# Kernel tuning notes

Measured on AMD Instinct MI355X. Metric: run time of the kernel, lower is better.

Reference implementation:

```python
import jax, jax.numpy as jnp
import numpy as np

N = 100000       # total_nodes
E = 400000       # total_events (event == E, all events used)
EMBED = 128
HIDDEN = 128
CLASSES = 10
Q = 4096         # query pairs for link prediction
BN_EPS = 1e-5


def _bn(x):
    # BatchNorm1d(affine=False), training mode: biased variance over batch dim
    m = jnp.mean(x, axis=0)
    var = jnp.var(x, axis=0)
    return (x - m) * jax.lax.rsqrt(var + BN_EPS)


def _t2_layer(h, u, v, g, w1, w2):
    # per-edge source features: [h[dst-side], g]  -> scatter_add into (N, F)
    src_u = jnp.concatenate([h[u], g], axis=1)   # (E, F)
    src_v = jnp.concatenate([h[v], g], axis=1)   # (E, F)
    F = src_u.shape[1]
    agg = (jnp.zeros((N, F), h.dtype)
           .at[v].add(src_u)
           .at[u].add(src_v))                    # agg_u + agg_v fused
    z = jax.nn.relu(_bn(agg) @ w1.T)             # (N, F)
    return jnp.concatenate([h, z], axis=1) @ w2.T  # (N, F + prev_embed)


def setup_inputs() -> dict:
    key = jax.random.key(0)
    ks = jax.random.split(key, 14)
    s = 0.05
    return {
        "u": jax.random.randint(ks[0], (E,), 0, N, dtype=jnp.int32),
        "v": jax.random.randint(ks[1], (E,), 0, N, dtype=jnp.int32),
        "t": jnp.sort(jax.random.uniform(ks[2], (E,), dtype=jnp.float32)),
        "qu": jax.random.randint(ks[3], (Q,), 0, N, dtype=jnp.int32),
        "qv": jax.random.randint(ks[4], (Q,), 0, N, dtype=jnp.int32),
        "h0": jax.random.uniform(ks[5], (N, EMBED), dtype=jnp.float32),
        "w1_0": jax.random.normal(ks[6], (129, 129), jnp.float32) * s,
        "w2_0": jax.random.normal(ks[7], (257, 257), jnp.float32) * s,
        "w1_1": jax.random.normal(ks[8], (258, 258), jnp.float32) * s,
        "w2_1": jax.random.normal(ks[9], (515, 515), jnp.float32) * s,
        "link_h": jax.random.normal(ks[10], (HIDDEN, 2 * 515), jnp.float32) * s,
        "link_o": jax.random.normal(ks[11], (1, HIDDEN), jnp.float32) * s,
        "node_h": jax.random.normal(ks[12], (HIDDEN, 515), jnp.float32) * s,
        "node_o": jax.random.normal(ks[13], (CLASSES, HIDDEN), jnp.float32) * s,
    }


def reference(u, v, t, qu, qv, h0, w1_0, w2_0, w1_1, w2_1,
              link_h, link_o, node_h, node_o):
    # g = (tlast - t) / (1 + tlast - tfirst), shape (E, 1)
    g = ((t[-1] - t) / (1.0 + t[-1] - t[0]))[:, None]
    h = _t2_layer(h0, u, v, g, w1_0, w2_0)   # (N, 257)
    h = _t2_layer(h, u, v, g, w1_1, w2_1)    # (N, 515)
    # link prediction head on query pairs
    hq = jnp.concatenate([h[qu], h[qv]], axis=1)            # (Q, 1030)
    link = (jax.nn.relu(hq @ link_h.T) @ link_o.T)[:, 0]    # (Q,)
    # node prediction head
    node = jax.nn.relu(h @ node_h.T) @ node_o.T             # (N, CLASSES)
    return link, node
```

## Files before the change

kernel.cpp:

```cpp
#include <hip/hip_runtime.h>
#include <hip/hip_bf16.h>

#define NN      100000
#define EE      400000
#define QQ      4096
#define CLASSES 10
#define BN_EPS  1e-5f
#define NCHUNK  256

typedef __hip_bfloat16 bf16;
typedef __attribute__((ext_vector_type(8))) short short8v;
typedef __attribute__((ext_vector_type(4))) float float4v;

__device__ inline float ldv(const float* p, long i) { return p[i]; }
__device__ inline float ldv(const bf16*  p, long i) { return __bfloat162float(p[i]); }
__device__ inline void  stv(float* p, long i, float v) { p[i] = v; }
__device__ inline void  stv(bf16*  p, long i, float v) { p[i] = __float2bfloat16(v); }

__device__ inline unsigned short f2b(float f) { bf16 b = __float2bfloat16(f); unsigned short s; __builtin_memcpy(&s, &b, 2); return s; }
__device__ inline float b2f(unsigned short s) { bf16 b; __builtin_memcpy(&b, &s, 2); return __bfloat162float(b); }

__device__ __forceinline__ void gload_lds16(const void* g, void* l) {
    __builtin_amdgcn_global_load_lds(
        (const __attribute__((address_space(1))) void*)g,
        (__attribute__((address_space(3))) void*)l,
        16, 0, 0);
}

__global__ void zero_kernel(float* __restrict__ p, size_t n) {
    size_t i  = (size_t)blockIdx.x * blockDim.x + threadIdx.x;
    size_t st = (size_t)gridDim.x * blockDim.x;
    for (; i < n; i += st) p[i] = 0.f;
}

__global__ void csr_count_kernel(const int* __restrict__ u, const int* __restrict__ v, int E, int* __restrict__ deg) {
    int e = blockIdx.x * 256 + threadIdx.x;
    if (e < E) { atomicAdd(&deg[u[e]], 1); atomicAdd(&deg[v[e]], 1); }
}

__global__ __launch_bounds__(256) void csr_chunksum_kernel(const int* __restrict__ deg, int N, int chunk, int* __restrict__ bsum) {
    __shared__ int sh[256];
    int b = blockIdx.x, tid = threadIdx.x;
    int i0 = b * chunk, i1 = min(N, i0 + chunk);
    int s = 0;
    for (int i = i0 + tid; i < i1; i += 256) s += deg[i];
    sh[tid] = s; __syncthreads();
    for (int st = 128; st > 0; st >>= 1) { if (tid < st) sh[tid] += sh[tid + st]; __syncthreads(); }
    if (tid == 0) bsum[b] = sh[0];
}

__global__ void csr_scanb_kernel(const int* __restrict__ bsum, int* __restrict__ boff) {
    if (threadIdx.x == 0 && blockIdx.x == 0) {
        int r = 0;
        for (int i = 0; i < NCHUNK; ++i) { boff[i] = r; r += bsum[i]; }
    }
}

__global__ void csr_rowp_kernel(const int* __restrict__ deg, const int* __restrict__ boff,
                                int N, int chunk, int* __restrict__ rowp, int* __restrict__ cur) {
    int b = blockIdx.x;
    if (threadIdx.x != 0) return;
    int i0 = b * chunk, i1 = min(N, i0 + chunk);
    int r = boff[b];
    for (int i = i0; i < i1; ++i) { rowp[i] = r; cur[i] = r; r += deg[i]; }
    if (b == NCHUNK - 1) rowp[N] = r;
}

__global__ void csr_fill_kernel(const int* __restrict__ u, const int* __restrict__ v,
                                const float* __restrict__ t, int E,
                                int* __restrict__ cur, int* __restrict__ adj, float* __restrict__ gsum) {
    int e = blockIdx.x * 256 + threadIdx.x;
    if (e >= E) return;
    int a = u[e], b = v[e];
    float tlast = t[E - 1], tfirst = t[0];
    float ge = (tlast - t[e]) / (1.0f + tlast - tfirst);
    int p = atomicAdd(&cur[a], 1); adj[p] = b;
    int q = atomicAdd(&cur[b], 1); adj[q] = a;
    atomicAdd(&gsum[a], ge); atomicAdd(&gsum[b], ge);
}

__global__ __launch_bounds__(256) void gather_l1_kernel(
    const float* __restrict__ h0, const int* __restrict__ rowp, const int* __restrict__ adj,
    const float* __restrict__ gsum, bf16* __restrict__ out, int N)
{
    int n = blockIdx.x * 4 + (threadIdx.x >> 6);
    if (n >= N) return;
    int lane = threadIdx.x & 63;
    float a0 = 0.f, a1 = 0.f;
    int j0 = rowp[n], j1 = rowp[n + 1];
    for (int j = j0; j < j1; ++j) {
        int o = adj[j];
        const float2 x = *(const float2*)(h0 + (long)o * 128 + 2 * lane);
        a0 += x.x; a1 += x.y;
    }
    bf16* orow = out + (long)n * 136;
    ushort2 pv; pv.x = f2b(a0); pv.y = f2b(a1);
    ((ushort2*)orow)[lane] = pv;
    if (lane == 0) {
        orow[128] = __float2bfloat16(gsum[n]);
        orow[129] = __float2bfloat16(0.f);
    } else if (lane < 4) {
        ushort2 z; z.x = 0; z.y = 0;
        ((ushort2*)(orow + 130))[lane - 1] = z;
    }
}

__global__ __launch_bounds__(256) void gather_l2_kernel(
    const bf16* __restrict__ h1, const int* __restrict__ rowp, const int* __restrict__ adj,
    const float* __restrict__ gsum, bf16* __restrict__ out, int N)
{
    int n = blockIdx.x * 4 + (threadIdx.x >> 6);
    if (n >= N) return;
    int lane = threadIdx.x & 63;
    float a0 = 0.f, a1 = 0.f, b0 = 0.f, b1 = 0.f, cS = 0.f;
    int j0 = rowp[n], j1 = rowp[n + 1];
    for (int j = j0; j < j1; ++j) {
        int o = adj[j];
        const ushort2* hr = (const ushort2*)(h1 + (long)o * 264);
        ushort2 x = hr[lane];
        ushort2 y = hr[64 + lane];
        a0 += b2f(x.x); a1 += b2f(x.y);
        b0 += b2f(y.x); b1 += b2f(y.y);
        if (lane == 0) cS += __bfloat162float(h1[(long)o * 264 + 256]);
    }
    bf16* orow = out + (long)n * 264;
    ushort2 p0; p0.x = f2b(a0); p0.y = f2b(a1);
    ushort2 p1; p1.x = f2b(b0); p1.y = f2b(b1);
    ((ushort2*)orow)[lane] = p0;
    ((ushort2*)orow)[64 + lane] = p1;
    if (lane == 0) {
        orow[256] = __float2bfloat16(cS);
        orow[257] = __float2bfloat16(gsum[n]);
    } else if (lane < 4) {
        ushort2 z; z.x = 0; z.y = 0;
        ((ushort2*)orow)[128 + lane] = z;
    }
}

__global__ __launch_bounds__(256) void col_stats_b_kernel(
    const bf16* __restrict__ X, int ld, int Nrows, int F,
    float* __restrict__ sum, float* __restrict__ sumsq)
{
    int tid = threadIdx.x;
    int rpb = (Nrows + gridDim.x - 1) / gridDim.x;
    int r0 = blockIdx.x * rpb, r1 = min(Nrows, r0 + rpb);
    int c0 = tid, c1 = tid + 256;
    float s0 = 0.f, q0 = 0.f, s1 = 0.f, q1 = 0.f;
    for (int r = r0; r < r1; ++r) {
        const bf16* row = X + (long)r * ld;
        if (c0 < F) { float x = __bfloat162float(row[c0]); s0 += x; q0 += x * x; }
        if (c1 < F) { float x = __bfloat162float(row[c1]); s1 += x; q1 += x * x; }
    }
    if (c0 < F) { atomicAdd(&sum[c0], s0); atomicAdd(&sumsq[c0], q0); }
    if (c1 < F) { atomicAdd(&sum[c1], s1); atomicAdd(&sumsq[c1], q1); }
}

__global__ void bn_finalize_kernel(const float* __restrict__ sum, const float* __restrict__ sumsq,
                                   int F, float Nf, float* __restrict__ mean, float* __restrict__ scale)
{
    int c = blockIdx.x * blockDim.x + threadIdx.x;
    if (c < F) {
        float m = sum[c] / Nf;
        float var = sumsq[c] / Nf - m * m;
        mean[c] = m;
        scale[c] = 1.0f / sqrtf(var + BN_EPS);
    }
}

__global__ __launch_bounds__(256) void wfold_kernel(
    const float* __restrict__ w, int Ktot, int M,
    const float* __restrict__ mean, const float* __restrict__ scale,
    int Kpad, int Mpad, bf16* __restrict__ wout, float* __restrict__ bias)
{
    __shared__ float sh[256];
    int m = blockIdx.x;
    int tid = threadIdx.x;
    float bs = 0.f;
    bf16* orow = wout + (long)m * Kpad;
    for (int k = tid; k < Kpad; k += 256) {
        float val = 0.f;
        if (m < M && k < Ktot) {
            float wv = w[(long)m * Ktot + k];
            val = wv * scale[k];
            bs -= mean[k] * scale[k] * wv;
        }
        orow[k] = __float2bfloat16(val);
    }
    sh[tid] = bs; __syncthreads();
    for (int st = 128; st > 0; st >>= 1) { if (tid < st) sh[tid] += sh[tid + st]; __syncthreads(); }
    if (tid == 0 && m < M) bias[m] = sh[0];
}

__global__ void wprep_kernel(const float* __restrict__ w, int Ktot, int M,
                             int K1, int W1, int K2, int Kpad, int Mpad,
                             bf16* __restrict__ out)
{
    int idx = blockIdx.x * 256 + threadIdx.x;
    if (idx >= Mpad * Kpad) return;
    int m = idx / Kpad, k = idx - m * Kpad;
    float val = 0.f;
    if (m < M) {
        if (k < W1) { if (k < K1) val = w[(long)m * Ktot + k]; }
        else { int j = k - W1; if (j < K2) val = w[(long)m * Ktot + K1 + j]; }
    }
    out[idx] = __float2bfloat16(val);
}

template<typename CT>
__global__ __launch_bounds__(256) void mfma_gemm_kernel(
    const bf16* __restrict__ A0, int lda0, int W1,
    const bf16* __restrict__ A1, int lda1,
    const bf16* __restrict__ Wb, int Kpad,
    const float* __restrict__ bias,
    CT* __restrict__ C, long ldc, int Nrows, int M, int padlim, int relu)
{
    __shared__ bf16 sA[128 * 32];
    __shared__ bf16 sB[128 * 32];

    int tid  = threadIdx.x;
    int row0 = blockIdx.x * 128;
    int col0 = blockIdx.y * 128;
    int wave = tid >> 6, lane = tid & 63;
    int wr = (wave >> 1) * 64, wc = (wave & 1) * 64;
    int la = lane & 15, hk = lane >> 4;

    float4v acc[4][4];
    #pragma unroll
    for (int i = 0; i < 4; ++i)
        #pragma unroll
        for (int j = 0; j < 4; ++j)
            acc[i][j] = (float4v){0.f, 0.f, 0.f, 0.f};

    const short8v* sA8 = (const short8v*)sA;
    const short8v* sB8 = (const short8v*)sB;

    for (int k0 = 0; k0 < Kpad; k0 += 32) {
        #pragma unroll
        for (int h = 0; h < 2; ++h) {
            int c = tid + h * 256;
            int r = c >> 2, kq = c & 3;
            int ka = k0 + kq * 8;
            int ga_row = row0 + r; if (ga_row >= Nrows) ga_row = Nrows - 1;
            const bf16* gp = (ka < W1) ? (A0 + (long)ga_row * lda0 + ka)
                                       : (A1 + (long)ga_row * lda1 + (ka - W1));
            gload_lds16(gp, (char*)sA + (size_t)c * 16);
            const bf16* gq = Wb + (long)(col0 + r) * Kpad + ka;
            gload_lds16(gq, (char*)sB + (size_t)c * 16);
        }
        __syncthreads();

        short8v afr[4], bfr[4];
        #pragma unroll
        for (int mf = 0; mf < 4; ++mf)
            afr[mf] = sA8[(size_t)(wr + mf * 16 + la) * 4 + hk];
        #pragma unroll
        for (int nf = 0; nf < 4; ++nf)
            bfr[nf] = sB8[(size_t)(wc + nf * 16 + la) * 4 + hk];
        #pragma unroll
        for (int mf = 0; mf < 4; ++mf)
            #pragma unroll
            for (int nf = 0; nf < 4; ++nf)
                acc[mf][nf] = __builtin_amdgcn_mfma_f32_16x16x32_bf16(
                    afr[mf], bfr[nf], acc[mf][nf], 0, 0, 0);
        __syncthreads();
    }

    #pragma unroll
    for (int mf = 0; mf < 4; ++mf) {
        #pragma unroll
        for (int r = 0; r < 4; ++r) {
            long grow = row0 + wr + mf * 16 + hk * 4 + r;
            if (grow >= Nrows) continue;
            #pragma unroll
            for (int nf = 0; nf < 4; ++nf) {
                int gcol = col0 + wc + nf * 16 + la;
                if (gcol >= padlim) continue;
                float vv = 0.f;
                if (gcol < M) {
                    vv = acc[mf][nf][r];
                    if (bias) vv += bias[gcol];
                    if (relu) vv = fmaxf(vv, 0.f);
                }
                stv(C, grow * ldc + gcol, vv);
            }
        }
    }
}

__global__ __launch_bounds__(256) void link_gather_kernel(
    const bf16* __restrict__ h2, const int* __restrict__ qu, const int* __restrict__ qv,
    bf16* __restrict__ hq)
{
    int q = blockIdx.x * 4 + (threadIdx.x >> 6);
    if (q >= QQ) return;
    int lane = threadIdx.x & 63;
    const ushort4* ra4 = (const ushort4*)(h2 + (long)qu[q] * 520);
    const ushort4* rb4 = (const ushort4*)(h2 + (long)qv[q] * 520);
    ushort4* o4 = (ushort4*)(hq + (long)q * 1056);
    #pragma unroll 3
    for (int k = lane; k < 130; k += 64) o4[k] = ra4[k];
    #pragma unroll 3
    for (int k = lane; k < 130; k += 64) o4[130 + k] = rb4[k];
    if (lane < 4) { ushort4 z; z.x = z.y = z.z = z.w = 0; o4[260 + lane] = z; }
}

__global__ __launch_bounds__(256) void link_dot_kernel(
    const float* __restrict__ tmpl, const float* __restrict__ link_o, float* __restrict__ out)
{
    int q = blockIdx.x * 4 + (threadIdx.x >> 6);
    if (q >= QQ) return;
    int lane = threadIdx.x & 63;
    const float* r = tmpl + (long)q * 128;
    float s = r[lane] * link_o[lane] + r[lane + 64] * link_o[lane + 64];
    #pragma unroll
    for (int off = 32; off > 0; off >>= 1) s += __shfl_xor(s, off, 64);
    if (lane == 0) out[q] = s;
}

template<typename HT>
__global__ __launch_bounds__(256) void scatter_edges_kernel(
    const HT* __restrict__ h, int ldh, int P,
    const int* __restrict__ u, const int* __restrict__ v,
    const float* __restrict__ t, int E,
    float* __restrict__ agg, int lda)
{
    long gid = (long)blockIdx.x * blockDim.x + threadIdx.x;
    int e = (int)(gid >> 6);
    int lane = (int)(gid & 63);
    if (e >= E) return;
    int uu = u[e], vv = v[e];
    float tlast = t[E - 1], tfirst = t[0];
    float ge = (tlast - t[e]) / (1.0f + tlast - tfirst);
    const HT* hu = h + (long)uu * ldh;
    const HT* hv = h + (long)vv * ldh;
    float* au = agg + (long)uu * lda;
    float* av = agg + (long)vv * lda;
    for (int f = lane; f < P; f += 64) {
        atomicAdd(&av[f], ldv(hu, f));
        atomicAdd(&au[f], ldv(hv, f));
    }
    if (lane == 0) {
        atomicAdd(&av[P], ge);
        atomicAdd(&au[P], ge);
    }
}

__global__ __launch_bounds__(256) void col_stats_kernel(
    const float* __restrict__ X, int Nrows, int F,
    float* __restrict__ sum, float* __restrict__ sumsq)
{
    int tid = threadIdx.x;
    int rowsPerBlock = (Nrows + gridDim.x - 1) / gridDim.x;
    int r0 = blockIdx.x * rowsPerBlock;
    int r1 = min(Nrows, r0 + rowsPerBlock);
    int c0 = tid, c1 = tid + 256;
    float s0 = 0.f, q0 = 0.f, s1 = 0.f, q1 = 0.f;
    for (int r = r0; r < r1; ++r) {
        const float* row = X + (long)r * F;
        if (c0 < F) { float x = row[c0]; s0 += x; q0 += x * x; }
        if (c1 < F) { float x = row[c1]; s1 += x; q1 += x * x; }
    }
    if (c0 < F) { atomicAdd(&sum[c0], s0); atomicAdd(&sumsq[c0], q0); }
    if (c1 < F) { atomicAdd(&sum[c1], s1); atomicAdd(&sumsq[c1], q1); }
}

#define BM 64
#define BNT 64
#define BK 32
template<typename AT0, typename AT1, typename CT>
__global__ __launch_bounds__(256) void gemm_kernel(
    const AT0* __restrict__ A0, int lda0, int cols0,
    const AT1* __restrict__ A1, int lda1,
    const float* __restrict__ Bw,
    CT* __restrict__ C, int ldc,
    int Nrows, int K, int M,
    const float* __restrict__ bn_mean, const float* __restrict__ bn_scale,
    int relu)
{
    __shared__ float sA[BM][BK + 1];
    __shared__ float sB[BNT][BK + 1];
    int row0 = blockIdx.x * BM;
    int col0 = blockIdx.y * BNT;
    int tid = threadIdx.x;
    int tx = tid & 15, ty = tid >> 4;
    float acc[4][4] = {{0.f}};
    for (int k0 = 0; k0 < K; k0 += BK) {
        int i = tid >> 2;
        int j = (tid & 3) * 8;
        int gr = row0 + i;
        int gm = col0 + i;
        #pragma unroll
        for (int s = 0; s < 8; ++s) {
            int gk = k0 + j + s;
            float val = 0.f;
            if (gr < Nrows && gk < K) {
                if (gk < cols0) val = ldv(A0, (long)gr * lda0 + gk);
                else            val = ldv(A1, (long)gr * lda1 + (gk - cols0));
                if (bn_mean) val = (val - bn_mean[gk]) * bn_scale[gk];
            }
            sA[i][j + s] = val;
            float bv = 0.f;
            if (gm < M && gk < K) bv = Bw[(long)gm * K + gk];
            sB[i][j + s] = bv;
        }
        __syncthreads();
        #pragma unroll
        for (int kk = 0; kk < BK; ++kk) {
            float a[4], b[4];
            #pragma unroll
            for (int r = 0; r < 4; ++r) a[r] = sA[ty * 4 + r][kk];
            #pragma unroll
            for (int c = 0; c < 4; ++c) b[c] = sB[tx * 4 + c][kk];
            #pragma unroll
            for (int r = 0; r < 4; ++r)
                #pragma unroll
                for (int c = 0; c < 4; ++c)
                    acc[r][c] += a[r] * b[c];
        }
        __syncthreads();
    }
    #pragma unroll
    for (int r = 0; r < 4; ++r) {
        int gr = row0 + ty * 4 + r;
        if (gr >= Nrows) continue;
        #pragma unroll
        for (int c = 0; c < 4; ++c) {
            int gm = col0 + tx * 4 + c;
            if (gm >= M) continue;
            float vv = acc[r][c];
            if (relu) vv = fmaxf(vv, 0.f);
            stv(C, (long)gr * ldc + gm, vv);
        }
    }
}

template<typename HT>
__global__ __launch_bounds__(128) void link_kernel(
    const HT* __restrict__ h2, int ldh,
    const int* __restrict__ qu, const int* __restrict__ qv,
    const float* __restrict__ link_h,
    const float* __restrict__ link_o,
    float* __restrict__ out)
{
    __shared__ float sh[1030];
    __shared__ float red[128];
    int q = blockIdx.x;
    int tid = threadIdx.x;
    int a = qu[q], b = qv[q];
    for (int k = tid; k < 515; k += 128) sh[k] = ldv(h2, (long)a * ldh + k);
    for (int k = tid; k < 515; k += 128) sh[515 + k] = ldv(h2, (long)b * ldh + k);
    __syncthreads();
    const float* wrow = link_h + (long)tid * 1030;
    float y = 0.f;
    for (int k = 0; k < 1030; ++k) y += sh[k] * wrow[k];
    y = fmaxf(y, 0.f) * link_o[tid];
    red[tid] = y;
    __syncthreads();
    for (int s = 64; s > 0; s >>= 1) {
        if (tid < s) red[tid] += red[tid + s];
        __syncthreads();
    }
    if (tid == 0) out[q] = red[0];
}

extern "C" void kernel_launch(void* const* d_in, const int* in_sizes, int n_in,
                              void* d_out, int out_size, void* d_ws, size_t ws_size,
                              hipStream_t stream)
{
    const int*   u      = (const int*)d_in[0];
    const int*   v      = (const int*)d_in[1];
    const float* t      = (const float*)d_in[2];
    const int*   qu     = (const int*)d_in[3];
    const int*   qv     = (const int*)d_in[4];
    const float* h0     = (const float*)d_in[5];
    const float* w1_0   = (const float*)d_in[6];
    const float* w2_0   = (const float*)d_in[7];
    const float* w1_1   = (const float*)d_in[8];
    const float* w2_1   = (const float*)d_in[9];
    const float* link_h = (const float*)d_in[10];
    const float* link_o = (const float*)d_in[11];
    const float* node_h = (const float*)d_in[12];
    const float* node_o = (const float*)d_in[13];

    float* out_link = (float*)d_out;
    float* out_node = (float*)d_out + QQ;

    char* wsb = (char*)d_ws;

    float* stats = (float*)wsb;
    float* sum1 = stats,         * sumsq1 = stats + 512;
    float* mean1 = stats + 1024, * scale1 = stats + 1536;
    float* sum2 = stats + 2048,  * sumsq2 = stats + 2560;
    float* mean2 = stats + 3072, * scale2 = stats + 3584;

    if (ws_size >= 217000000ull) {
        bf16* wf1_0 = (bf16*)(wsb + 16384);
        bf16* wb2_0 = (bf16*)(wsb + 98304);
        bf16* wf1_1 = (bf16*)(wsb + 319488);
        bf16* wb2_1 = (bf16*)(wsb + 540672);
        bf16* wbnh  = (bf16*)(wsb + 1236992);
        bf16* wbno  = (bf16*)(wsb + 1376256);
        float* bias1 = (float*)(wsb + 1409024);
        float* bias2 = (float*)(wsb + 1410048);
        float* gsum = (float*)(wsb + 1412096);
        int*   deg  = (int*)  (wsb + 1812096);
        int*   rowp = (int*)  (wsb + 2212096);
        int*   cur  = (int*)  (wsb + 2612104);
        int*   bsum = (int*)  (wsb + 3012104);
        int*   boff = (int*)  (wsb + 3013128);
        int*   adj  = (int*)  (wsb + 3016200);
        bf16*  wlk  = (bf16*) (wsb + 6220000);
        bf16* h1   = (bf16*)(wsb + 6500000ull);
        bf16* tmpb = (bf16*)(wsb + 6500000ull);
        bf16* z0   = (bf16*)(wsb + 59300000ull);
        bf16* h0b  = (bf16*)(wsb + 86500000ull);
        bf16* z1   = (bf16*)(wsb + 59300000ull);
        bf16* hq   = (bf16*)(wsb + 59300000ull);
        float* tmpl = (float*)(wsb + 70000000ull);
        bf16* aggb = (bf16*)(wsb + 112100000ull);
        bf16* h2   = (bf16*)(wsb + 112100000ull);

        const int gx = (NN + 127) / 128;
        const int chunk = (NN + NCHUNK - 1) / NCHUNK;

        zero_kernel<<<16, 256, 0, stream>>>(stats, 4096);
        zero_kernel<<<64, 256, 0, stream>>>(gsum, 200000);

        wprep_kernel<<<432, 256, 0, stream>>>(w2_0, 257, 257, 128, 128, 129, 288, 384, wb2_0);
        wprep_kernel<<<1360, 256, 0, stream>>>(w2_1, 515, 515, 257, 272, 258, 544, 640, wb2_1);
        wprep_kernel<<<272, 256, 0, stream>>>(node_h, 515, 128, 515, 544, 0, 544, 128, wbnh);
        wprep_kernel<<<64, 256, 0, stream>>>(node_o, 128, 10, 128, 128, 0, 128, 128, wbno);
        wprep_kernel<<<528, 256, 0, stream>>>(link_h, 1030, 128, 515, 520, 515, 1056, 128, wlk);

        csr_count_kernel<<<(EE + 255) / 256, 256, 0, stream>>>(u, v, EE, deg);
        csr_chunksum_kernel<<<NCHUNK, 256, 0, stream>>>(deg, NN, chunk, bsum);
        csr_scanb_kernel<<<1, 64, 0, stream>>>(bsum, boff);
        csr_rowp_kernel<<<NCHUNK, 64, 0, stream>>>(deg, boff, NN, chunk, rowp, cur);
        csr_fill_kernel<<<(EE + 255) / 256, 256, 0, stream>>>(u, v, t, EE, cur, adj, gsum);

        gather_l1_kernel<<<NN / 4, 256, 0, stream>>>(h0, rowp, adj, gsum, aggb, NN);
        col_stats_b_kernel<<<512, 256, 0, stream>>>(aggb, 136, NN, 129, sum1, sumsq1);
        bn_finalize_kernel<<<2, 256, 0, stream>>>(sum1, sumsq1, 129, (float)NN, mean1, scale1);
        wfold_kernel<<<256, 256, 0, stream>>>(w1_0, 129, 129, mean1, scale1, 160, 256, wf1_0, bias1);
        mfma_gemm_kernel<bf16><<<dim3(gx, 2), 256, 0, stream>>>(
            aggb, 136, 160, aggb, 136, wf1_0, 160, bias1, z0, 136, NN, 129, 136, 1);
        wprep_kernel<<<50000, 256, 0, stream>>>(h0, 128, NN, 128, 128, 0, 128, NN, h0b);
        mfma_gemm_kernel<bf16><<<dim3(gx, 3), 256, 0, stream>>>(
            h0b, 128, 128, z0, 136, wb2_0, 288, nullptr, h1, 264, NN, 257, 264, 0);

        gather_l2_kernel<<<NN / 4, 256, 0, stream>>>(h1, rowp, adj, gsum, aggb, NN);
        col_stats_b_kernel<<<512, 256, 0, stream>>>(aggb, 264, NN, 258, sum2, sumsq2);
        bn_finalize_kernel<<<2, 256, 0, stream>>>(sum2, sumsq2, 258, (float)NN, mean2, scale2);
        wfold_kernel<<<384, 256, 0, stream>>>(w1_1, 258, 258, mean2, scale2, 288, 384, wf1_1, bias2);
        mfma_gemm_kernel<bf16><<<dim3(gx, 3), 256, 0, stream>>>(
            aggb, 264, 288, aggb, 264, wf1_1, 288, bias2, z1, 264, NN, 258, 264, 1);
        mfma_gemm_kernel<bf16><<<dim3(gx, 5), 256, 0, stream>>>(
            h1, 264, 272, z1, 264, wb2_1, 544, nullptr, h2, 520, NN, 515, 520, 0);

        mfma_gemm_kernel<bf16><<<dim3(gx, 1), 256, 0, stream>>>(
            h2, 520, 544, h2, 520, wbnh, 544, nullptr, tmpb, 128, NN, 128, 128, 1);
        mfma_gemm_kernel<float><<<dim3(gx, 1), 256, 0, stream>>>(
            tmpb, 128, 128, tmpb, 128, wbno, 128, nullptr, out_node, CLASSES, NN, 10, 10, 0);

        link_gather_kernel<<<QQ / 4, 256, 0, stream>>>(h2, qu, qv, hq);
        mfma_gemm_kernel<float><<<dim3(QQ / 128, 1), 256, 0, stream>>>(
            hq, 1056, 1056, hq, 1056, wlk, 1056, nullptr, tmpl, 128, QQ, 128, 128, 1);
        link_dot_kernel<<<QQ / 4, 256, 0, stream>>>(tmpl, link_o, out_link);
    } else {
        const int gx = (NN + BM - 1) / BM;
        const int scatter_blocks = (EE * 64 + 255) / 256;
        float* agg = (float*)(wsb + 16384);
        bf16*  h2b = (bf16*) (wsb + 16384);
        bf16*  h1b = (bf16*) (wsb + 16384 + 103200000ull);
        bf16*  zb  = (bf16*) (wsb + 16384 + 154600000ull);
        float* tmp = (float*)(wsb + 16384 + 154600000ull);

        zero_kernel<<<16, 256, 0, stream>>>(stats, 4096);

        zero_kernel<<<2048, 256, 0, stream>>>(agg, (size_t)NN * 129);
        scatter_edges_kernel<float><<<scatter_blocks, 256, 0, stream>>>(
            h0, 128, 128, u, v, t, EE, agg, 129);
        col_stats_kernel<<<512, 256, 0, stream>>>(agg, NN, 129, sum1, sumsq1);
        bn_finalize_kernel<<<2, 256, 0, stream>>>(sum1, sumsq1, 129, (float)NN, mean1, scale1);
        gemm_kernel<float, float, bf16><<<dim3(gx, 3), 256, 0, stream>>>(
            agg, 129, 129, (const float*)nullptr, 0, w1_0, zb, 129, NN, 129, 129, mean1, scale1, 1);
        gemm_kernel<float, bf16, bf16><<<dim3(gx, 5), 256, 0, stream>>>(
            h0, 128, 128, zb, 129, w2_0, h1b, 257, NN, 257, 257, nullptr, nullptr, 0);

        zero_kernel<<<2048, 256, 0, stream>>>(agg, (size_t)NN * 258);
        scatter_edges_kernel<bf16><<<scatter_blocks, 256, 0, stream>>>(
            h1b, 257, 257, u, v, t, EE, agg, 258);
        col_stats_kernel<<<512, 256, 0, stream>>>(agg, NN, 258, sum2, sumsq2);
        bn_finalize_kernel<<<2, 256, 0, stream>>>(sum2, sumsq2, 258, (float)NN, mean2, scale2);
        gemm_kernel<float, float, bf16><<<dim3(gx, 5), 256, 0, stream>>>(
            agg, 258, 258, (const float*)nullptr, 0, w1_1, zb, 258, NN, 258, 258, mean2, scale2, 1);
        gemm_kernel<bf16, bf16, bf16><<<dim3(gx, 9), 256, 0, stream>>>(
            h1b, 257, 257, zb, 258, w2_1, h2b, 515, NN, 515, 515, nullptr, nullptr, 0);

        gemm_kernel<bf16, float, float><<<dim3(gx, 2), 256, 0, stream>>>(
            h2b, 515, 515, (const float*)nullptr, 0, node_h, tmp, 128, NN, 515, 128, nullptr, nullptr, 1);
        gemm_kernel<float, float, float><<<dim3(gx, 1), 256, 0, stream>>>(
            tmp, 128, 128, tmp, 128, node_o, out_node, CLASSES, NN, 128, CLASSES, nullptr, nullptr, 0);

        link_kernel<bf16><<<QQ, 128, 0, stream>>>(h2b, 515, qu, qv, link_h, link_o, out_link);
    }
}
```

Baseline: 1.089 ms.

## Gather layer-1 from bf16 features, remap GEMM grid, hoist load offsets

Moves the h0-to-bf16 conversion ahead of the layer-1 neighbor gather so the gather reads half-width rows instead of fp32 rows. The GEMM launch becomes a 1D grid with the column tile varying fastest, so blocks sharing an A row tile run adjacently and can reuse it in cache. Per-iteration address arithmetic in the GEMM load loop is precomputed outside the K loop. Gathering bf16 inputs changes layer-1 aggregation numerics slightly, since values are rounded before summation.

```diff
diff --git a/kernel.cpp b/kernel.cpp
--- a/kernel.cpp
+++ b/kernel.cpp
@@ -80,7 +80,7 @@
 }
 
 __global__ __launch_bounds__(256) void gather_l1_kernel(
-    const float* __restrict__ h0, const int* __restrict__ rowp, const int* __restrict__ adj,
+    const bf16* __restrict__ h0b, const int* __restrict__ rowp, const int* __restrict__ adj,
     const float* __restrict__ gsum, bf16* __restrict__ out, int N)
 {
     int n = blockIdx.x * 4 + (threadIdx.x >> 6);
@@ -90,8 +90,8 @@
     int j0 = rowp[n], j1 = rowp[n + 1];
     for (int j = j0; j < j1; ++j) {
         int o = adj[j];
-        const float2 x = *(const float2*)(h0 + (long)o * 128 + 2 * lane);
-        a0 += x.x; a1 += x.y;
+        ushort2 x = ((const ushort2*)(h0b + (long)o * 128))[lane];
+        a0 += b2f(x.x); a1 += b2f(x.y);
     }
     bf16* orow = out + (long)n * 136;
     ushort2 pv; pv.x = f2b(a0); pv.y = f2b(a1);
@@ -212,14 +212,15 @@
     const bf16* __restrict__ A1, int lda1,
     const bf16* __restrict__ Wb, int Kpad,
     const float* __restrict__ bias,
-    CT* __restrict__ C, long ldc, int Nrows, int M, int padlim, int relu)
+    CT* __restrict__ C, long ldc, int Nrows, int M, int padlim, int relu, int gy)
 {
     __shared__ bf16 sA[128 * 32];
     __shared__ bf16 sB[128 * 32];
 
     int tid  = threadIdx.x;
-    int row0 = blockIdx.x * 128;
-    int col0 = blockIdx.y * 128;
+    int bid  = blockIdx.x;
+    int row0 = (bid / gy) * 128;
+    int col0 = (bid % gy) * 128;
     int wave = tid >> 6, lane = tid & 63;
     int wr = (wave >> 1) * 64, wc = (wave & 1) * 64;
     int la = lane & 15, hk = lane >> 4;
@@ -234,18 +235,30 @@
     const short8v* sA8 = (const short8v*)sA;
     const short8v* sB8 = (const short8v*)sB;
 
+    long offA0[2], offA1[2], offW[2];
+    int  kq8_[2];
+    char *ldsA_[2], *ldsB_[2];
+    #pragma unroll
+    for (int h = 0; h < 2; ++h) {
+        int c = tid + h * 256;
+        int r = c >> 2;
+        int kq8 = (c & 3) * 8;
+        kq8_[h] = kq8;
+        int ga_row = row0 + r; if (ga_row >= Nrows) ga_row = Nrows - 1;
+        offA0[h] = (long)ga_row * lda0 + kq8;
+        offA1[h] = (long)ga_row * lda1 + kq8 - W1;
+        offW[h]  = (long)(col0 + r) * Kpad + kq8;
+        ldsA_[h] = (char*)sA + (size_t)c * 16;
+        ldsB_[h] = (char*)sB + (size_t)c * 16;
+    }
+
     for (int k0 = 0; k0 < Kpad; k0 += 32) {
         #pragma unroll
         for (int h = 0; h < 2; ++h) {
-            int c = tid + h * 256;
-            int r = c >> 2, kq = c & 3;
-            int ka = k0 + kq * 8;
-            int ga_row = row0 + r; if (ga_row >= Nrows) ga_row = Nrows - 1;
-            const bf16* gp = (ka < W1) ? (A0 + (long)ga_row * lda0 + ka)
-                                       : (A1 + (long)ga_row * lda1 + (ka - W1));
-            gload_lds16(gp, (char*)sA + (size_t)c * 16);
-            const bf16* gq = Wb + (long)(col0 + r) * Kpad + ka;
-            gload_lds16(gq, (char*)sB + (size_t)c * 16);
+            int ka = k0 + kq8_[h];
+            const bf16* gp = (ka < W1) ? (A0 + offA0[h] + k0) : (A1 + offA1[h] + k0);
+            gload_lds16(gp, ldsA_[h]);
+            gload_lds16(Wb + offW[h] + k0, ldsB_[h]);
         }
         __syncthreads();
 
@@ -301,7 +314,7 @@
     for (int k = lane; k < 130; k += 64) o4[k] = ra4[k];
     #pragma unroll 3
     for (int k = lane; k < 130; k += 64) o4[130 + k] = rb4[k];
-    if (lane < 4) { ushort4 z; z.x = z.y = z.z = z.w = 0; o4[260 + lane] = z; }
+    if (lane < 4) { ushort4 z; z.x = z.y = z.z = z.w = 0; o4[260 + lane] = z;}
 }
 
 __global__ __launch_bounds__(256) void link_dot_kernel(
@@ -531,6 +544,7 @@
         wprep_kernel<<<272, 256, 0, stream>>>(node_h, 515, 128, 515, 544, 0, 544, 128, wbnh);
         wprep_kernel<<<64, 256, 0, stream>>>(node_o, 128, 10, 128, 128, 0, 128, 128, wbno);
         wprep_kernel<<<528, 256, 0, stream>>>(link_h, 1030, 128, 515, 520, 515, 1056, 128, wlk);
+        wprep_kernel<<<50000, 256, 0, stream>>>(h0, 128, NN, 128, 128, 0, 128, NN, h0b);
 
         csr_count_kernel<<<(EE + 255) / 256, 256, 0, stream>>>(u, v, EE, deg);
         csr_chunksum_kernel<<<NCHUNK, 256, 0, stream>>>(deg, NN, chunk, bsum);
@@ -538,33 +552,32 @@
         csr_rowp_kernel<<<NCHUNK, 64, 0, stream>>>(deg, boff, NN, chunk, rowp, cur);
         csr_fill_kernel<<<(EE + 255) / 256, 256, 0, stream>>>(u, v, t, EE, cur, adj, gsum);
 
-        gather_l1_kernel<<<NN / 4, 256, 0, stream>>>(h0, rowp, adj, gsum, aggb, NN);
+        gather_l1_kernel<<<NN / 4, 256, 0, stream>>>(h0b, rowp, adj, gsum, aggb, NN);
         col_stats_b_kernel<<<512, 256, 0, stream>>>(aggb, 136, NN, 129, sum1, sumsq1);
         bn_finalize_kernel<<<2, 256, 0, stream>>>(sum1, sumsq1, 129, (float)NN, mean1, scale1);
         wfold_kernel<<<256, 256, 0, stream>>>(w1_0, 129, 129, mean1, scale1, 160, 256, wf1_0, bias1);
-        mfma_gemm_kernel<bf16><<<dim3(gx, 2), 256, 0, stream>>>(
-            aggb, 136, 160, aggb, 136, wf1_0, 160, bias1, z0, 136, NN, 129, 136, 1);
-        wprep_kernel<<<50000, 256, 0, stream>>>(h0, 128, NN, 128, 128, 0, 128, NN, h0b);
-        mfma_gemm_kernel<bf16><<<dim3(gx, 3), 256, 0, stream>>>(
-            h0b, 128, 128, z0, 136, wb2_0, 288, nullptr, h1, 264, NN, 257, 264, 0);
+        mfma_gemm_kernel<bf16><<<gx * 2, 256, 0, stream>>>(
+            aggb, 136, 160, aggb, 136, wf1_0, 160, bias1, z0, 136, NN, 129, 136, 1, 2);
+        mfma_gemm_kernel<bf16><<<gx * 3, 256, 0, stream>>>(
+            h0b, 128, 128, z0, 136, wb2_0, 288, nullptr, h1, 264, NN, 257, 264, 0, 3);
 
         gather_l2_kernel<<<NN / 4, 256, 0, stream>>>(h1, rowp, adj, gsum, aggb, NN);
         col_stats_b_kernel<<<512, 256, 0, stream>>>(aggb, 264, NN, 258, sum2, sumsq2);
         bn_finalize_kernel<<<2, 256, 0, stream>>>(sum2, sumsq2, 258, (float)NN, mean2, scale2);
         wfold_kernel<<<384, 256, 0, stream>>>(w1_1, 258, 258, mean2, scale2, 288, 384, wf1_1, bias2);
-        mfma_gemm_kernel<bf16><<<dim3(gx, 3), 256, 0, stream>>>(
-            aggb, 264, 288, aggb, 264, wf1_1, 288, bias2, z1, 264, NN, 258, 264, 1);
-        mfma_gemm_kernel<bf16><<<dim3(gx, 5), 256, 0, stream>>>(
-            h1, 264, 272, z1, 264, wb2_1, 544, nullptr, h2, 520, NN, 515, 520, 0);
-
-        mfma_gemm_kernel<bf16><<<dim3(gx, 1), 256, 0, stream>>>(
-            h2, 520, 544, h2, 520, wbnh, 544, nullptr, tmpb, 128, NN, 128, 128, 1);
-        mfma_gemm_kernel<float><<<dim3(gx, 1), 256, 0, stream>>>(
-            tmpb, 128, 128, tmpb, 128, wbno, 128, nullptr, out_node, CLASSES, NN, 10, 10, 0);
+        mfma_gemm_kernel<bf16><<<gx * 3, 256, 0, stream>>>(
+            aggb, 264, 288, aggb, 264, wf1_1, 288, bias2, z1, 264, NN, 258, 264, 1, 3);
+        mfma_gemm_kernel<bf16><<<gx * 5, 256, 0, stream>>>(
+            h1, 264, 272, z1, 264, wb2_1, 544, nullptr, h2, 520, NN, 515, 520, 0, 5);
+
+        mfma_gemm_kernel<bf16><<<gx, 256, 0, stream>>>(
+            h2, 520, 544, h2, 520, wbnh, 544, nullptr, tmpb, 128, NN, 128, 128, 1, 1);
+        mfma_gemm_kernel<float><<<gx, 256, 0, stream>>>(
+            tmpb, 128, 128, tmpb, 128, wbno, 128, nullptr, out_node, CLASSES, NN, 10, 10, 0, 1);
 
         link_gather_kernel<<<QQ / 4, 256, 0, stream>>>(h2, qu, qv, hq);
-        mfma_gemm_kernel<float><<<dim3(QQ / 128, 1), 256, 0, stream>>>(
-            hq, 1056, 1056, hq, 1056, wlk, 1056, nullptr, tmpl, 128, QQ, 128, 128, 1);
+        mfma_gemm_kernel<float><<<QQ / 128, 256, 0, stream>>>(
+            hq, 1056, 1056, hq, 1056, wlk, 1056, nullptr, tmpl, 128, QQ, 128, 128, 1, 1);
         link_dot_kernel<<<QQ / 4, 256, 0, stream>>>(tmpl, link_o, out_link);
     } else {
         const int gx = (NN + BM - 1) / BM;
```

Result: no change. 1.107 ms (+1.6%).
